# Kernel tuning notes

Hardware: AMD Instinct MI355X
Metric: run time of the kernel (lower is better)

The kernel has to match this reference:

```python
import jax, jax.numpy as jnp
import numpy as np

B, S, I, H = 128, 1024, 512, 1024


def setup_inputs() -> dict:
    key = jax.random.key(0)
    k0, k1, k2 = jax.random.split(key, 3)
    scale = 0.02
    return {
        "x": jax.random.normal(k0, (B, S, I), jnp.float32),
        "feature_weighting": jnp.ones((1, 1, I), jnp.float32),
        "temporal_weighting": jnp.ones((1, S, 1), jnp.float32),
        "magnitude": jnp.ones((1,), jnp.float32),
        "W0": jax.random.normal(k1, (3 * H, I + H), jnp.float32) * scale,
        "b0": jnp.zeros((3 * H,), jnp.float32),
        "W1": jax.random.normal(k2, (3 * H, 2 * H), jnp.float32) * scale,
        "b1": jnp.zeros((3 * H,), jnp.float32),
    }


def _cell(x_t, h_prev, c_prev, W, b):
    # gates: [B, 3H] from cat(x, h_prev) @ W.T + b
    gates = jnp.concatenate([x_t, h_prev], axis=1) @ W.T + b
    i, g, o = jnp.split(gates, 3, axis=1)
    f = jax.nn.sigmoid(c_prev)            # note: forget gate from c_prev (module's quirk)
    c_new = f * c_prev + jax.nn.sigmoid(i) * jnp.tanh(g)
    h_new = jax.nn.sigmoid(o) * jnp.tanh(c_new) * f  # extra *f (module's quirk)
    return h_new, c_new


def reference(x, feature_weighting, temporal_weighting, magnitude, W0, b0, W1, b1):
    batch = x.shape[0]
    hid = W0.shape[0] // 3
    x = x * feature_weighting * temporal_weighting * jnp.exp(magnitude)
    zeros = jnp.zeros((batch, hid), x.dtype)
    init = (zeros, zeros, zeros, zeros)  # h0, c0, h1, c1

    def step(carry, x_t):
        h0, c0, h1, c1 = carry
        h0, c0 = _cell(x_t, h0, c0, W0, b0)
        h1, c1 = _cell(h0, h1, c1, W1, b1)
        return (h0, c0, h1, c1), h1

    (h0, c0, h1, c1), ys = jax.lax.scan(step, init, jnp.swapaxes(x, 0, 1))
    outputs = jnp.swapaxes(ys, 0, 1)  # [B, S, H]
    return outputs, ((h0, c0), (h1, c1))
```

## Files before the change

kernel.cpp:

```cpp
#include <hip/hip_runtime.h>
#include <hip/hip_bf16.h>


typedef __attribute__((ext_vector_type(8))) _Float16 f16x8;
typedef __attribute__((ext_vector_type(4))) float f32x4;
typedef unsigned long long u64;
#define DEV __device__ __forceinline__

namespace {
constexpr int Bb = 128, Ss = 1024, Ii = 512, Hh = 1024;
constexpr int K0 = Ii + Hh;
constexpr int K1 = 2 * Hh;
constexpr int NWG = 256;
constexpr int NPH = Ss + 1;
constexpr int RING = 8;
constexpr int SSTR = 32;

constexpr size_t BH    = (size_t)Bb * Hh;
constexpr size_t OF_H0 = (size_t)Bb * Ss * Hh;
constexpr size_t OF_C0 = OF_H0 + BH;
constexpr size_t OF_H1 = OF_C0 + BH;
constexpr size_t OF_C1 = OF_H1 + BH;

constexpr size_t WS_GO    = 0;
constexpr size_t WS_SLOTS = 4096;
constexpr size_t WS_C0    = 40960;
constexpr size_t WS_C1    = WS_C0 + BH * 4;
constexpr size_t RINGF    = (size_t)RING * BH * 2;
constexpr size_t WS_H0F   = WS_C1 + BH * 4;
constexpr size_t WS_H1F   = WS_H0F + RINGF;
constexpr size_t WS_ZEND  = WS_H1F + RINGF;
constexpr size_t WSZ_W0   = (size_t)3 * Hh * K0 * 2;
constexpr size_t WSZ_W1   = (size_t)3 * Hh * K1 * 2;
constexpr size_t WS_W0F   = WS_ZEND;
constexpr size_t WS_W1F   = WS_W0F + WSZ_W0;
constexpr size_t WS_NEED  = WS_W1F + WSZ_W1;

constexpr int CHUNKB    = 3072;
constexpr int LO_BYTES  = 48 * CHUNKB;
constexpr int RED_BYTES = 4 * 3 * 64 * 16;
constexpr int DYN_LDS   = LO_BYTES + RED_BYTES;
}

DEV unsigned short f16b(float f) {
  return __builtin_bit_cast(unsigned short, (_Float16)f);
}
DEV float sig_(float x) { return 1.f / (1.f + __expf(-x)); }
DEV float tanh_(float x) {
  float e = __expf(-2.f * fabsf(x));
  return copysignf((1.f - e) / (1.f + e), x);
}
DEV f16x8 ldh(const unsigned short* p) { return *reinterpret_cast<const f16x8*>(p); }
#define MFMAH __builtin_amdgcn_mfma_f32_16x16x32_f16

__global__ void k_zero(uint4* p, int n16) {
  for (int i = blockIdx.x * blockDim.x + threadIdx.x; i < n16; i += gridDim.x * blockDim.x)
    p[i] = make_uint4(0u, 0u, 0u, 0u);
}

__global__ void k_convert(const float* __restrict__ W0, const float* __restrict__ W1,
                          unsigned short* __restrict__ w0f, unsigned short* __restrict__ w1f) {
  const long NW04 = (long)3 * Hh * K0 / 4;
  const long NW14 = (long)3 * Hh * K1 / 4;
  const long total = NW04 + NW14;
  for (long i = (long)blockIdx.x * blockDim.x + threadIdx.x; i < total;
       i += (long)gridDim.x * blockDim.x) {
    long e; const float* src; unsigned short* dst;
    if (i < NW04) { e = i * 4;          src = W0 + e; dst = w0f + e; }
    else          { e = (i - NW04) * 4; src = W1 + e; dst = w1f + e; }
    f32x4 v = *(const f32x4*)src;
    u64 pk = 0;
#pragma unroll
    for (int e2 = 0; e2 < 4; ++e2) pk |= (u64)f16b(v[e2]) << (16 * e2);
    *(u64*)dst = pk;
  }
}

#define LD_W(g, kl)                                                           \
  (*(const f16x8*)(lds + ((kl) >> 5) * CHUNKB + (g) * 1024 + l4 * 256 + l15 * 16))

#define HLOAD(arr, n, hP, kaB)                                                \
  _Pragma("unroll") for (int c_ = 0; c_ < (n); ++c_)                          \
    arr[c_] = ldh((hP) + (kaB) + c_ * 32);

#define HCOMP(arr, n, koB)                                                    \
  _Pragma("unroll") for (int c_ = 0; c_ < (n); ++c_) {                        \
    const int ko_ = (koB) + c_ * 32;                                          \
    f32x4 &I_ = (c_ & 1) ? aI1 : aI0;                                         \
    f32x4 &G_ = (c_ & 1) ? aG1 : aG0;                                         \
    f32x4 &O_ = (c_ & 1) ? aO1 : aO0;                                         \
    I_ = MFMAH(LD_W(0, ko_), arr[c_], I_, 0, 0, 0);                           \
    G_ = MFMAH(LD_W(1, ko_), arr[c_], G_, 0, 0, 0);                           \
    O_ = MFMAH(LD_W(2, ko_), arr[c_], O_, 0, 0, 0);                           \
  }

#define WLOAD(a0, a1, a2, n, koB)                                             \
  _Pragma("unroll") for (int c_ = 0; c_ < (n); ++c_) {                        \
    const int ko_ = (koB) + c_ * 32;                                          \
    a0[c_] = ldh(wf + off0 + ko_);                                            \
    a1[c_] = ldh(wf + off1 + ko_);                                            \
    a2[c_] = ldh(wf + off2 + ko_);                                            \
  }

#define GCOMP(h_, a0, a1, a2, n)                                              \
  _Pragma("unroll") for (int c_ = 0; c_ < (n); ++c_) {                        \
    f32x4 &I_ = (c_ & 1) ? aI1 : aI0;                                         \
    f32x4 &G_ = (c_ & 1) ? aG1 : aG0;                                         \
    f32x4 &O_ = (c_ & 1) ? aO1 : aO0;                                         \
    I_ = MFMAH(a0[c_], h_[c_], I_, 0, 0, 0);                                  \
    G_ = MFMAH(a1[c_], h_[c_], G_, 0, 0, 0);                                  \
    O_ = MFMAH(a2[c_], h_[c_], O_, 0, 0, 0);                                  \
  }

#define XCOMP()                                                               \
  _Pragma("unroll") for (int c_ = 0; c_ < 16; ++c_) {                         \
    const int ko_ = c_ * 32;                                                  \
    f32x4 &I_ = (c_ & 1) ? aI1 : aI0;                                         \
    f32x4 &G_ = (c_ & 1) ? aG1 : aG0;                                         \
    f32x4 &O_ = (c_ & 1) ? aO1 : aO0;                                         \
    I_ = MFMAH(LD_W(0, ko_), xp[c_], I_, 0, 0, 0);                            \
    G_ = MFMAH(LD_W(1, ko_), xp[c_], G_, 0, 0, 0);                            \
    O_ = MFMAH(LD_W(2, ko_), xp[c_], O_, 0, 0, 0);                            \
  }

#define XPREF(tn)                                                             \
  do {                                                                        \
    const float* pxn_ = xf + ((size_t)bact * Ss + (tn)) * Ii + l4 * 8;        \
    const float twn_ = tw[tn] * emag;                                         \
    _Pragma("unroll") for (int c_ = 0; c_ < 16; ++c_) {                       \
      const int k_ = c_ * 32;                                                 \
      f32x4 a0_ = *(const f32x4*)(pxn_ + k_);                                 \
      f32x4 a1_ = *(const f32x4*)(pxn_ + k_ + 4);                             \
      f32x4 b0_ = *(const f32x4*)(fw + k_ + l4 * 8);                          \
      f32x4 b1_ = *(const f32x4*)(fw + k_ + l4 * 8 + 4);                      \
      a0_ *= b0_ * twn_; a1_ *= b1_ * twn_;                                   \
      _Pragma("unroll") for (int e_ = 0; e_ < 4; ++e_) {                      \
        xp[c_][e_] = (_Float16)a0_[e_];                                       \
        xp[c_][e_ + 4] = (_Float16)a1_[e_];                                   \
      }                                                                       \
    }                                                                         \
  } while (0)

__global__ __launch_bounds__(512, 2) void lstm_persist(
    const float* __restrict__ xf,
    const float* __restrict__ fw, const float* __restrict__ tw, const float* __restrict__ mag,
    const unsigned short* __restrict__ w0f, const float* __restrict__ b0,
    const unsigned short* __restrict__ w1f, const float* __restrict__ b1,
    float* __restrict__ out,
    unsigned short* __restrict__ h0f, unsigned short* __restrict__ h1f,
    float* __restrict__ c0, float* __restrict__ c1,
    int* __restrict__ slots, int* __restrict__ go) {
  extern __shared__ char lds[];
  f32x4* red = reinterpret_cast<f32x4*>(lds + LO_BYTES);

  const int tid = threadIdx.x;
  const int lane = tid & 63;
  const int wv = tid >> 6;
  const int mt = wv & 3;
  const int kh = wv >> 2;
  const int l15 = lane & 15, l4 = lane >> 4;

  const int wg = blockIdx.x;
  const int layer = wg >> 7;
  const int i = wg & 127;
  const int x8 = i & 7;
  const int kk = i >> 3;
  const int mg = x8 >> 2;
  const int jt = (x8 & 3) * 16 + kk;
  const int jb = jt * 16;

  const int bact = mg * 64 + mt * 16 + l15;
  const int j0 = jb + l4 * 4;

  const int K = layer ? K1 : K0;
  const unsigned short* wf = layer ? w1f : w0f;
  const size_t off0 = (size_t)(0 * Hh + jb + l15) * K + l4 * 8;
  const size_t off1 = (size_t)(1 * Hh + jb + l15) * K + l4 * 8;
  const size_t off2 = (size_t)(2 * Hh + jb + l15) * K + l4 * 8;

  const float* bb = layer ? b1 : b0;
  const f32x4 bi = *(const f32x4*)(bb + j0);
  const f32x4 bg = *(const f32x4*)(bb + Hh + j0);
  const f32x4 bo = *(const f32x4*)(bb + 2 * Hh + j0);

  float* cst = (layer ? c1 : c0) + (size_t)bact * Hh + j0;
  float* outb = out + (size_t)bact * Ss * Hh + j0;
  const float emag = __expf(mag[0]);

  {
    const u64* wsl = (const u64*)wf;
    const int K4 = K >> 2;
    for (int idx = tid; idx < 48 * 384; idx += 512) {
      int R = idx / 384;
      int o = idx - R * 384;
      int g = R >> 4, rr = R & 15;
      u64 v = wsl[(size_t)(g * Hh + jb + rr) * K4 + o];
      *(u64*)(lds + (o >> 3) * CHUNKB + g * 1024 + ((o >> 1) & 3) * 256 +
              rr * 16 + (o & 1) * 8) = v;
    }
  }
  f16x8 xp[16];
  if (layer == 0 && kh == 0) XPREF(0);
  __syncthreads();

  for (int p = 0; p < NPH; ++p) {
    const bool act = layer ? (p >= 1) : (p < Ss);
    const int t = layer ? (p - 1) : p;
    const int rslot = (p - 1) & (RING - 1);
    const int wslot = p & (RING - 1);

    if (act) {
      f32x4 z = {0.f, 0.f, 0.f, 0.f};
      f32x4 aI0 = z, aG0 = z, aO0 = z, aI1 = z, aG1 = z, aO1 = z;
      const unsigned short* h0r = h0f + (size_t)rslot * BH + (size_t)bact * Hh + l4 * 8;
      const unsigned short* h1r = h1f + (size_t)rslot * BH + (size_t)bact * Hh + l4 * 8;

      if (layer == 0) {
        if (kh == 0) {
          f16x8 hA[12];
          HLOAD(hA, 12, h0r, 0);
          XCOMP();
          HCOMP(hA, 12, Ii);
        } else {
          f16x8 hA[10], hB[10];
          HLOAD(hA, 10, h0r, 384);
          HLOAD(hB, 10, h0r, 704);
          HCOMP(hA, 10, Ii + 384);
          HCOMP(hB, 10, Ii + 704);
        }
      } else {
        if (kh == 0) {
          f16x8 g0[12], g1[12], g2a[8], g2b[4], g3[12];
          HLOAD(g0, 12, h0r, 0);
          HLOAD(g1, 12, h0r, 384);
          HCOMP(g0, 12, 0);
          HLOAD(g2a, 8, h0r, 768);
          HLOAD(g2b, 4, h1r, 0);
          HCOMP(g1, 12, 384);
          HLOAD(g3, 12, h1r, 128);
          HCOMP(g2a, 8, 768);
          HCOMP(g2b, 4, Hh);
          HCOMP(g3, 12, Hh + 128);
        } else {
          {
            f16x8 sh[6], sA[6], sB[6], sC[6];
            HLOAD(sh, 6, h1r, 512);
            WLOAD(sA, sB, sC, 6, Hh + 512);
            GCOMP(sh, sA, sB, sC, 6);
          }
          {
            f16x8 sh[6], sA[6], sB[6], sC[6];
            HLOAD(sh, 6, h1r, 704);
            WLOAD(sA, sB, sC, 6, Hh + 704);
            GCOMP(sh, sA, sB, sC, 6);
          }
          {
            f16x8 sh[4], sA[4], sB[4], sC[4];
            HLOAD(sh, 4, h1r, 896);
            WLOAD(sA, sB, sC, 4, Hh + 896);
            GCOMP(sh, sA, sB, sC, 4);
          }
        }
      }

      if (kh == 1) {
        red[((mt * 3 + 0) << 6) + lane] = aI0 + aI1;
        red[((mt * 3 + 1) << 6) + lane] = aG0 + aG1;
        red[((mt * 3 + 2) << 6) + lane] = aO0 + aO1;
      }
      __syncthreads();
      if (kh == 0) {
        f32x4 ai = aI0 + aI1 + red[((mt * 3 + 0) << 6) + lane] + bi;
        f32x4 ag = aG0 + aG1 + red[((mt * 3 + 1) << 6) + lane] + bg;
        f32x4 ao = aO0 + aO1 + red[((mt * 3 + 2) << 6) + lane] + bo;
        f32x4 cp = *(const f32x4*)cst;
        f32x4 cn, hn;
        u64 hpk = 0;
#pragma unroll
        for (int r = 0; r < 4; ++r) {
          float f = sig_(cp[r]);
          float cc = f * cp[r] + sig_(ai[r]) * tanh_(ag[r]);
          float hh = sig_(ao[r]) * tanh_(cc) * f;
          cn[r] = cc; hn[r] = hh;
          hpk |= (u64)f16b(hh) << (16 * r);
        }
        *(f32x4*)cst = cn;
        const size_t wbase = (size_t)wslot * BH + (size_t)bact * Hh + j0;
        __hip_atomic_store((u64*)((layer ? h1f : h0f) + wbase), hpk,
                           __ATOMIC_RELAXED, __HIP_MEMORY_SCOPE_AGENT);
        if (layer) {
          *(f32x4*)(outb + (size_t)t * Hh) = hn;
          if (t == Ss - 1) {
            *(f32x4*)(out + OF_H1 + (size_t)bact * Hh + j0) = hn;
            *(f32x4*)(out + OF_C1 + (size_t)bact * Hh + j0) = cn;
          }
        } else if (t == Ss - 1) {
          *(f32x4*)(out + OF_H0 + (size_t)bact * Hh + j0) = hn;
          *(f32x4*)(out + OF_C0 + (size_t)bact * Hh + j0) = cn;
        }
      }
      if (layer == 0 && kh == 0 && t + 1 < Ss) XPREF(t + 1);
    }

    if (p < NPH - 1) {
      __syncthreads();
      if (wg == 0) {
        if (tid == 0)
          __hip_atomic_store(&slots[0], p + 1, __ATOMIC_RELAXED, __HIP_MEMORY_SCOPE_AGENT);
        int gd = 0; bool ok;
        do {
          ok = true;
          if (tid < 256)
            ok = __hip_atomic_load(&slots[tid * SSTR], __ATOMIC_RELAXED,
                                   __HIP_MEMORY_SCOPE_AGENT) > p;
          if (!ok) __builtin_amdgcn_s_sleep(1);
        } while (!__syncthreads_and(ok) && ++gd < (1 << 22));
        if (tid < 8)
          __hip_atomic_store(&go[tid * SSTR], p + 1, __ATOMIC_RELAXED,
                             __HIP_MEMORY_SCOPE_AGENT);
      } else {
        if (tid == 0) {
          __hip_atomic_store(&slots[wg * SSTR], p + 1, __ATOMIC_RELAXED,
                             __HIP_MEMORY_SCOPE_AGENT);
          int gd = 0;
          while (__hip_atomic_load(&go[x8 * SSTR], __ATOMIC_RELAXED,
                                   __HIP_MEMORY_SCOPE_AGENT) <= p &&
                 ++gd < (1 << 24))
            __builtin_amdgcn_s_sleep(1);
        }
        __syncthreads();
      }
      if ((p & (RING - 1)) == (RING - 1)) {
        if (tid == 0) __builtin_amdgcn_fence(__ATOMIC_ACQUIRE, "agent");
        __syncthreads();
      }
    }
  }
}

extern "C" void kernel_launch(void* const* d_in, const int* in_sizes, int n_in,
                              void* d_out, int out_size, void* d_ws, size_t ws_size,
                              hipStream_t stream) {
  const float* x   = (const float*)d_in[0];
  const float* fw  = (const float*)d_in[1];
  const float* tw  = (const float*)d_in[2];
  const float* mag = (const float*)d_in[3];
  const float* W0  = (const float*)d_in[4];
  const float* b0  = (const float*)d_in[5];
  const float* W1  = (const float*)d_in[6];
  const float* b1  = (const float*)d_in[7];
  float* out = (float*)d_out;
  char* ws = (char*)d_ws;

  if (ws_size < WS_NEED) return;

  unsigned short* w0f = (unsigned short*)(ws + WS_W0F);
  unsigned short* w1f = (unsigned short*)(ws + WS_W1F);

  (void)hipFuncSetAttribute((const void*)lstm_persist,
                            hipFuncAttributeMaxDynamicSharedMemorySize, DYN_LDS);

  k_zero<<<1290, 256, 0, stream>>>((uint4*)ws, (int)(WS_ZEND / 16));
  k_convert<<<1024, 256, 0, stream>>>(W0, W1, w0f, w1f);

  lstm_persist<<<NWG, 512, DYN_LDS, stream>>>(
      x, fw, tw, mag, w0f, b0, w1f, b1, out,
      (unsigned short*)(ws + WS_H0F), (unsigned short*)(ws + WS_H1F),
      (float*)(ws + WS_C0), (float*)(ws + WS_C1),
      (int*)(ws + WS_SLOTS), (int*)(ws + WS_GO));
}
```

Baseline: 16.93 ms.

## Replace centralized grid barrier with all-to-all polling and hoist x-projection off critical path

The master-workgroup barrier (wg0 gathers all slots, then broadcasts go flags) is replaced by a decentralized barrier where every workgroup polls all 256 slot counters itself, removing one round trip of cross-CU latency per timestep. The input-projection MFMA for step t+1 is now computed right after step t finishes, overlapping with barrier wait, and the h-work is rebalanced evenly between the two wave halves. The ring buffer grows to 16 slots and launch bounds change to 1 block per CU. The all-to-all polling raises traffic on the slot cache lines, and keeping x accumulators live across the barrier adds register pressure.

```diff
diff --git a/kernel.cpp b/kernel.cpp
--- a/kernel.cpp
+++ b/kernel.cpp
@@ -13,7 +13,7 @@
 constexpr int K1 = 2 * Hh;
 constexpr int NWG = 256;
 constexpr int NPH = Ss + 1;
-constexpr int RING = 8;
+constexpr int RING = 16;
 constexpr int SSTR = 32;
 
 constexpr size_t BH    = (size_t)Bb * Hh;
@@ -22,7 +22,6 @@
 constexpr size_t OF_H1 = OF_C0 + BH;
 constexpr size_t OF_C1 = OF_H1 + BH;
 
-constexpr size_t WS_GO    = 0;
 constexpr size_t WS_SLOTS = 4096;
 constexpr size_t WS_C0    = 40960;
 constexpr size_t WS_C1    = WS_C0 + BH * 4;
@@ -141,7 +140,10 @@
     }                                                                         \
   } while (0)
 
-__global__ __launch_bounds__(512, 2) void lstm_persist(
+#define ZACC() do { f32x4 z_ = {0.f,0.f,0.f,0.f};                             \
+    aI0 = z_; aG0 = z_; aO0 = z_; aI1 = z_; aG1 = z_; aO1 = z_; } while (0)
+
+__global__ __launch_bounds__(512, 1) void lstm_persist(
     const float* __restrict__ xf,
     const float* __restrict__ fw, const float* __restrict__ tw, const float* __restrict__ mag,
     const unsigned short* __restrict__ w0f, const float* __restrict__ b0,
@@ -149,7 +151,7 @@
     float* __restrict__ out,
     unsigned short* __restrict__ h0f, unsigned short* __restrict__ h1f,
     float* __restrict__ c0, float* __restrict__ c1,
-    int* __restrict__ slots, int* __restrict__ go) {
+    int* __restrict__ slots) {
   extern __shared__ char lds[];
   f32x4* red = reinterpret_cast<f32x4*>(lds + LO_BYTES);
 
@@ -171,6 +173,7 @@
 
   const int bact = mg * 64 + mt * 16 + l15;
   const int j0 = jb + l4 * 4;
+  const bool xwave = (layer == 0) && (kh == 0);
 
   const int K = layer ? K1 : K0;
   const unsigned short* wf = layer ? w1f : w0f;
@@ -199,9 +202,12 @@
               rr * 16 + (o & 1) * 8) = v;
     }
   }
+  __syncthreads();
+
+  f32x4 aI0, aG0, aO0, aI1, aG1, aO1;
+  ZACC();
   f16x8 xp[16];
-  if (layer == 0 && kh == 0) XPREF(0);
-  __syncthreads();
+  if (xwave) { XPREF(0); XCOMP(); }
 
   for (int p = 0; p < NPH; ++p) {
     const bool act = layer ? (p >= 1) : (p < Ss);
@@ -210,23 +216,23 @@
     const int wslot = p & (RING - 1);
 
     if (act) {
-      f32x4 z = {0.f, 0.f, 0.f, 0.f};
-      f32x4 aI0 = z, aG0 = z, aO0 = z, aI1 = z, aG1 = z, aO1 = z;
+      if (!xwave) ZACC();
       const unsigned short* h0r = h0f + (size_t)rslot * BH + (size_t)bact * Hh + l4 * 8;
       const unsigned short* h1r = h1f + (size_t)rslot * BH + (size_t)bact * Hh + l4 * 8;
 
       if (layer == 0) {
         if (kh == 0) {
-          f16x8 hA[12];
-          HLOAD(hA, 12, h0r, 0);
-          XCOMP();
-          HCOMP(hA, 12, Ii);
+          f16x8 hA[8], hB[8];
+          HLOAD(hA, 8, h0r, 0);
+          HLOAD(hB, 8, h0r, 256);
+          HCOMP(hA, 8, Ii);
+          HCOMP(hB, 8, Ii + 256);
         } else {
-          f16x8 hA[10], hB[10];
-          HLOAD(hA, 10, h0r, 384);
-          HLOAD(hB, 10, h0r, 704);
-          HCOMP(hA, 10, Ii + 384);
-          HCOMP(hB, 10, Ii + 704);
+          f16x8 hA[8], hB[8];
+          HLOAD(hA, 8, h0r, 512);
+          HLOAD(hB, 8, h0r, 768);
+          HCOMP(hA, 8, Ii + 512);
+          HCOMP(hB, 8, Ii + 768);
         }
       } else {
         if (kh == 0) {
@@ -299,37 +305,26 @@
           *(f32x4*)(out + OF_C0 + (size_t)bact * Hh + j0) = cn;
         }
       }
-      if (layer == 0 && kh == 0 && t + 1 < Ss) XPREF(t + 1);
+      if (xwave && t + 1 < Ss) {
+        XPREF(t + 1);
+        ZACC();
+        XCOMP();
+      }
     }
 
     if (p < NPH - 1) {
       __syncthreads();
-      if (wg == 0) {
-        if (tid == 0)
-          __hip_atomic_store(&slots[0], p + 1, __ATOMIC_RELAXED, __HIP_MEMORY_SCOPE_AGENT);
-        int gd = 0; bool ok;
-        do {
-          ok = true;
-          if (tid < 256)
-            ok = __hip_atomic_load(&slots[tid * SSTR], __ATOMIC_RELAXED,
-                                   __HIP_MEMORY_SCOPE_AGENT) > p;
-          if (!ok) __builtin_amdgcn_s_sleep(1);
-        } while (!__syncthreads_and(ok) && ++gd < (1 << 22));
-        if (tid < 8)
-          __hip_atomic_store(&go[tid * SSTR], p + 1, __ATOMIC_RELAXED,
-                             __HIP_MEMORY_SCOPE_AGENT);
-      } else {
-        if (tid == 0) {
-          __hip_atomic_store(&slots[wg * SSTR], p + 1, __ATOMIC_RELAXED,
-                             __HIP_MEMORY_SCOPE_AGENT);
-          int gd = 0;
-          while (__hip_atomic_load(&go[x8 * SSTR], __ATOMIC_RELAXED,
-                                   __HIP_MEMORY_SCOPE_AGENT) <= p &&
-                 ++gd < (1 << 24))
-            __builtin_amdgcn_s_sleep(1);
-        }
-        __syncthreads();
-      }
+      if (tid == 0)
+        __hip_atomic_store(&slots[wg * SSTR], p + 1, __ATOMIC_RELAXED,
+                           __HIP_MEMORY_SCOPE_AGENT);
+      bool ok = (tid >= 256);
+      int gd = 0;
+      do {
+        if (!ok)
+          ok = __hip_atomic_load(&slots[tid * SSTR], __ATOMIC_RELAXED,
+                                 __HIP_MEMORY_SCOPE_AGENT) > p;
+        if (!ok) __builtin_amdgcn_s_sleep(1);
+      } while (!__syncthreads_and(ok) && ++gd < (1 << 22));
       if ((p & (RING - 1)) == (RING - 1)) {
         if (tid == 0) __builtin_amdgcn_fence(__ATOMIC_ACQUIRE, "agent");
         __syncthreads();
@@ -360,12 +355,12 @@
   (void)hipFuncSetAttribute((const void*)lstm_persist,
                             hipFuncAttributeMaxDynamicSharedMemorySize, DYN_LDS);
 
-  k_zero<<<1290, 256, 0, stream>>>((uint4*)ws, (int)(WS_ZEND / 16));
+  k_zero<<<2048, 256, 0, stream>>>((uint4*)ws, (int)(WS_ZEND / 16));
   k_convert<<<1024, 256, 0, stream>>>(W0, W1, w0f, w1f);
 
   lstm_persist<<<NWG, 512, DYN_LDS, stream>>>(
       x, fw, tw, mag, w0f, b0, w1f, b1, out,
       (unsigned short*)(ws + WS_H0F), (unsigned short*)(ws + WS_H1F),
       (float*)(ws + WS_C0), (float*)(ws + WS_C1),
-      (int*)(ws + WS_SLOTS), (int*)(ws + WS_GO));
-}
+      (int*)(ws + WS_SLOTS));
+}
```

Measured after the change: 17.26 ms. No clear change (+1.9%).
